# Optimization experiments

Measured on AMD Instinct MI355X. Metric: run time of the kernel, lower is better.

The kernel has to match this reference:

```python
import jax, jax.numpy as jnp
import numpy as np

N, E, D, ETYPES = 20000, 200000, 256, 16

def _gelu(x):
    return jax.nn.gelu(x, approximate=False)

def setup_inputs() -> dict:
    key = jax.random.key(0)
    ks = jax.random.split(key, 24)
    s = lambda k, shape, fan: (jax.random.normal(k, shape, jnp.float32) / np.sqrt(fan)).astype(jnp.float32)
    inp = {}
    inp['node_embeddings'] = jax.random.normal(ks[0], (N, D), jnp.float32)
    inp['edge_index'] = jax.random.randint(ks[1], (2, E), 0, N, jnp.int64 if jax.config.jax_enable_x64 else jnp.int32)
    inp['edge_type'] = jax.random.randint(ks[2], (E,), 0, ETYPES, jnp.int32)
    inp['task_embedding'] = jax.random.normal(ks[3], (D,), jnp.float32)
    inp['edge_emb'] = s(ks[4], (ETYPES, D), D)
    inp['msg_W'] = s(ks[5], (D, D), D); inp['msg_b'] = jnp.zeros((D,), jnp.float32)
    inp['att_W1'] = s(ks[6], (4 * D, D), 4 * D); inp['att_b1'] = jnp.zeros((D,), jnp.float32)
    inp['att_W2'] = s(ks[7], (D, 1), D); inp['att_b2'] = jnp.zeros((1,), jnp.float32)
    inp['edge_scale'] = jnp.asarray(0.5, jnp.float32)
    inp['ma_W1'] = s(ks[8], (D, 2 * D), D); inp['ma_b1'] = jnp.zeros((2 * D,), jnp.float32)
    inp['ma_W2'] = s(ks[9], (2 * D, 2 * D), 2 * D); inp['ma_b2'] = jnp.zeros((2 * D,), jnp.float32)
    inp['up_W1'] = s(ks[10], (2 * D, D), 2 * D); inp['up_b1'] = jnp.zeros((D,), jnp.float32)
    inp['up_W2'] = s(ks[11], (D, D), D); inp['up_b2'] = jnp.zeros((D,), jnp.float32)
    inp['ua_W1'] = s(ks[12], (D, 2 * D), D); inp['ua_b1'] = jnp.zeros((2 * D,), jnp.float32)
    inp['ua_W2'] = s(ks[13], (2 * D, 2 * D), 2 * D); inp['ua_b2'] = jnp.zeros((2 * D,), jnp.float32)
    inp['ln_g'] = jnp.ones((D,), jnp.float32); inp['ln_b'] = jnp.zeros((D,), jnp.float32)
    return inp

def reference(node_embeddings, edge_index, edge_type, task_embedding, edge_emb,
              msg_W, msg_b, att_W1, att_b1, att_W2, att_b2, edge_scale,
              ma_W1, ma_b1, ma_W2, ma_b2, up_W1, up_b1, up_W2, up_b2,
              ua_W1, ua_b1, ua_W2, ua_b2, ln_g, ln_b):
    n_nodes = node_embeddings.shape[0]
    src, dst = edge_index[0], edge_index[1]
    e = edge_emb[edge_type]                       # [E, D]
    x_src = node_embeddings[src]                  # [E, D]
    x_dst = node_embeddings[dst]                  # [E, D]
    messages = (x_src + e) @ msg_W + msg_b        # [E, D]
    # edge attention over [x_src, x_dst, edge_repr, task]
    task_rep = jnp.broadcast_to(task_embedding, (src.shape[0], task_embedding.shape[0]))
    att_in = jnp.concatenate([x_src, x_dst, e, task_rep], axis=-1)  # [E, 4D]
    edge_delta = jnp.tanh(_gelu(att_in @ att_W1 + att_b1) @ att_W2 + att_b2)  # [E, 1]
    edge_weight = 1.0 + edge_scale * edge_delta   # [E, 1]
    # FiLM-style message adapter from task embedding
    ma = _gelu(task_embedding @ ma_W1 + ma_b1) @ ma_W2 + ma_b2      # [2D]
    msg_gamma, msg_beta = ma[:ma.shape[0] // 2], ma[ma.shape[0] // 2:]
    messages = messages * (1.0 + 0.5 * jnp.tanh(msg_gamma)) + msg_beta
    messages = messages * edge_weight
    # scatter-add aggregation with degree normalization
    agg = jax.ops.segment_sum(messages, dst, num_segments=n_nodes)            # [N, D]
    deg = jax.ops.segment_sum(edge_weight[:, 0], dst, num_segments=n_nodes)   # [N]
    agg = agg / jnp.maximum(deg, 1.0)[:, None]
    ua = _gelu(task_embedding @ ua_W1 + ua_b1) @ ua_W2 + ua_b2      # [2D]
    upd_gamma, upd_beta = ua[:ua.shape[0] // 2], ua[ua.shape[0] // 2:]
    agg = agg * (1.0 + 0.5 * jnp.tanh(upd_gamma)) + upd_beta
    upd_in = jnp.concatenate([node_embeddings, agg], axis=-1)       # [N, 2D]
    updated = _gelu(upd_in @ up_W1 + up_b1) @ up_W2 + up_b2         # [N, D]
    y = node_embeddings + updated
    mu = jnp.mean(y, axis=-1, keepdims=True)
    var = jnp.mean((y - mu) ** 2, axis=-1, keepdims=True)
    return (y - mu) / jnp.sqrt(var + 1e-5) * ln_g + ln_b
```

## Files before the change

### kernel.cpp

```cpp
#include <hip/hip_runtime.h>
#include <hip/hip_bf16.h>

#define NN 20000
#define NE 200000

typedef __bf16 bf16x8 __attribute__((ext_vector_type(8)));
typedef float f32x4 __attribute__((ext_vector_type(4)));
typedef unsigned short u16x8 __attribute__((ext_vector_type(8)));

constexpr int TAB_MSG_SCALE = 0;
constexpr int TAB_MSG_BETA  = 256;
constexpr int TAB_UPD_SCALE = 512;
constexpr int TAB_UPD_BETA  = 768;
constexpr int TAB_TASKC     = 1024;
constexpr int TAB_ECM       = 1280;
constexpr size_t OFF_WPRET = 40960;
constexpr size_t OFF_W1T   = 434176;
constexpr size_t OFF_W2T   = 696320;
constexpr size_t OFF_CNT   = 827392;
constexpr size_t OFF_SRCET = 907392;
constexpr size_t OFF_UPDB  = 11147392;
constexpr size_t OFF_G     = 21387392;
constexpr size_t OFF_P2B   = 41867392;
constexpr size_t WS_NEED   = 52107392;

constexpr int ROW_BLOCKS = (NN + 63)/64;

__device__ __forceinline__ float bf2f(unsigned short u){
  union { unsigned int i; float f; } v; v.i = ((unsigned int)u) << 16; return v.f;
}
__device__ __forceinline__ unsigned short f2bf(float f){
  __bf16 h = (__bf16)f; unsigned short u; __builtin_memcpy(&u, &h, 2); return u;
}
__device__ __forceinline__ float gelu_f(float x){
  return 0.5f * x * (1.0f + erff(x * 0.70710678118654752f));
}
__device__ __forceinline__ float gelu_fast(float x){
  return x / (1.0f + __expf(-1.702f * x));
}
__device__ __forceinline__ float tanh_fast(float x){
  float e = __expf(2.0f * x);
  return 1.0f - 2.0f / (e + 1.0f);
}
__device__ __forceinline__ float sum16(const float* p){
  float a = ((p[0]+p[1])+(p[2]+p[3])) + ((p[4]+p[5])+(p[6]+p[7]));
  float b = ((p[8]+p[9])+(p[10]+p[11])) + ((p[12]+p[13])+(p[14]+p[15]));
  return a + b;
}

__global__ __launch_bounds__(256) void k_setup(
    const float* __restrict__ task, const float* __restrict__ eemb,
    const float* __restrict__ msg_W, const float* __restrict__ msg_b,
    const float* __restrict__ att_W1, const float* __restrict__ att_b1,
    const float* __restrict__ ma_W1, const float* __restrict__ ma_b1,
    const float* __restrict__ ma_W2, const float* __restrict__ ma_b2,
    const float* __restrict__ ua_W1, const float* __restrict__ ua_b1,
    const float* __restrict__ ua_W2, const float* __restrict__ ua_b2,
    const float* __restrict__ up_W1, const float* __restrict__ up_W2,
    const int* __restrict__ eidx, const int* __restrict__ etype,
    float* __restrict__ tabs,
    unsigned short* __restrict__ WpreT, unsigned short* __restrict__ W1T,
    unsigned short* __restrict__ W2T, int* __restrict__ cnt,
    unsigned int* __restrict__ srcet)
{
  __shared__ float s_in[512];
  __shared__ float s_h[512];
  int bb = blockIdx.x, tid = threadIdx.x;
  if (bb >= 1315){
    int e = (bb - 1315)*256 + tid;
    if (e < NE){
      int dst = eidx[NE + e];
      int pos = atomicAdd(&cnt[dst], 1);
      srcet[((unsigned)dst << 7) + pos] =
          (unsigned int)eidx[e] | ((unsigned int)etype[e] << 16);
    }
    return;
  }
  if (bb >= 35){
    int b = bb - 35;
    if (b < 768){
      int n = b;
      float v;
      if (n < 256)      v = msg_W[tid*256 + n];
      else if (n < 512) v = att_W1[tid*256 + (n - 256)];
      else              v = att_W1[(256 + tid)*256 + (n - 512)];
      WpreT[n*256 + tid] = f2bf(v);
    } else if (b < 1024){
      int n = b - 768;
      W1T[n*512 + tid]       = f2bf(up_W1[tid*256 + n]);
      W1T[n*512 + 256 + tid] = f2bf(up_W1[(256 + tid)*256 + n]);
    } else {
      int n = b - 1024;
      W2T[n*256 + tid] = f2bf(up_W2[tid*256 + n]);
    }
    return;
  }
  int b = bb;
  if (b < 2){
    const float* W1 = b ? ua_W1 : ma_W1;  const float* b1 = b ? ua_b1 : ma_b1;
    const float* W2 = b ? ua_W2 : ma_W2;  const float* b2 = b ? ua_b2 : ma_b2;
    s_in[tid] = task[tid];
    __syncthreads();
    #pragma unroll
    for (int jj = 0; jj < 2; ++jj){
      int j = tid + jj*256;
      float pacc[16];
      #pragma unroll
      for (int u = 0; u < 16; ++u) pacc[u] = 0.f;
      for (int k0 = 0; k0 < 256; k0 += 16){
        float wv[16];
        #pragma unroll
        for (int u = 0; u < 16; ++u) wv[u] = W1[(k0 + u)*512 + j];
        #pragma unroll
        for (int u = 0; u < 16; ++u) pacc[u] += s_in[k0 + u] * wv[u];
      }
      s_h[j] = gelu_f(b1[j] + sum16(pacc));
    }
    __syncthreads();
    float o[2];
    #pragma unroll
    for (int jj = 0; jj < 2; ++jj){
      int j = tid + jj*256;
      float pacc[16];
      #pragma unroll
      for (int u = 0; u < 16; ++u) pacc[u] = 0.f;
      for (int k0 = 0; k0 < 512; k0 += 16){
        float wv[16];
        #pragma unroll
        for (int u = 0; u < 16; ++u) wv[u] = W2[(k0 + u)*512 + j];
        #pragma unroll
        for (int u = 0; u < 16; ++u) pacc[u] += s_h[k0 + u] * wv[u];
      }
      o[jj] = b2[j] + sum16(pacc);
    }
    float* scale = tabs + (b ? TAB_UPD_SCALE : TAB_MSG_SCALE);
    float* beta  = tabs + (b ? TAB_UPD_BETA  : TAB_MSG_BETA);
    scale[tid] = 1.0f + 0.5f * tanhf(o[0]);
    beta[tid]  = o[1];
  } else if (b == 2){
    s_in[tid] = task[tid];
    __syncthreads();
    float pacc[16];
    #pragma unroll
    for (int u = 0; u < 16; ++u) pacc[u] = 0.f;
    for (int k0 = 0; k0 < 256; k0 += 16){
      float wv[16];
      #pragma unroll
      for (int u = 0; u < 16; ++u) wv[u] = att_W1[(768 + k0 + u)*256 + tid];
      #pragma unroll
      for (int u = 0; u < 16; ++u) pacc[u] += s_in[k0 + u] * wv[u];
    }
    tabs[TAB_TASKC + tid] = att_b1[tid] + sum16(pacc);
  } else if (b < 19){
    int t = b - 3;
    s_in[tid] = eemb[t*256 + tid];
    __syncthreads();
    float pacc[16];
    #pragma unroll
    for (int u = 0; u < 16; ++u) pacc[u] = 0.f;
    for (int k0 = 0; k0 < 256; k0 += 16){
      float wv[16];
      #pragma unroll
      for (int u = 0; u < 16; ++u) wv[u] = msg_W[(k0 + u)*256 + tid];
      #pragma unroll
      for (int u = 0; u < 16; ++u) pacc[u] += s_in[k0 + u] * wv[u];
    }
    tabs[TAB_ECM + t*512 + ((tid >> 2) << 3) + 4 + (tid & 3)] = msg_b[tid] + sum16(pacc);
  } else {
    int t = b - 19;
    s_in[tid] = eemb[t*256 + tid];
    __syncthreads();
    float pacc[16];
    #pragma unroll
    for (int u = 0; u < 16; ++u) pacc[u] = 0.f;
    for (int k0 = 0; k0 < 256; k0 += 16){
      float wv[16];
      #pragma unroll
      for (int u = 0; u < 16; ++u) wv[u] = att_W1[(512 + k0 + u)*256 + tid];
      #pragma unroll
      for (int u = 0; u < 16; ++u) pacc[u] += s_in[k0 + u] * wv[u];
    }
    tabs[TAB_ECM + t*512 + ((tid >> 2) << 3) + (tid & 3)] = sum16(pacc);
  }
}

__global__ __launch_bounds__(256) void k_gemm_pre(
    const float* __restrict__ X, const unsigned short* __restrict__ WpreT,
    const float* __restrict__ tabs,
    unsigned short* __restrict__ G, unsigned short* __restrict__ P2b)
{
  __shared__ __align__(16) unsigned short s_b[16*256];
  int tid = threadIdx.x;
  int bb = blockIdx.x;
  int rb = bb >> 2, chunk = bb & 3;
  int wv = tid >> 6, lane = tid & 63;
  int m0 = rb*64 + wv*16;
  bool valid = (m0 < NN);
  int lo = lane & 15, hi = lane >> 4;
  bf16x8 a[8];
  if (valid){
    const float* xrow = X + (size_t)(m0 + lo)*256 + hi*8;
    #pragma unroll
    for (int kc = 0; kc < 8; ++kc){
      float4 f0 = *(const float4*)(xrow + kc*32);
      float4 f1 = *(const float4*)(xrow + kc*32 + 4);
      bf16x8 v;
      v[0]=(__bf16)f0.x; v[1]=(__bf16)f0.y; v[2]=(__bf16)f0.z; v[3]=(__bf16)f0.w;
      v[4]=(__bf16)f1.x; v[5]=(__bf16)f1.y; v[6]=(__bf16)f1.z; v[7]=(__bf16)f1.w;
      a[kc] = v;
    }
  }
  int sn = tid >> 4, sk0 = (tid & 15)*16;
  int sswz = (sn & 7) << 3;
  int rswz = (lo & 7) << 3;
  for (int t = 0; t < 12; ++t){
    int nt = chunk*12 + t;
    __syncthreads();
    {
      const unsigned short* gsrc = WpreT + (size_t)(nt*16 + sn)*256 + sk0;
      uint4 d0 = *(const uint4*)(gsrc);
      uint4 d1 = *(const uint4*)(gsrc + 8);
      *(uint4*)(s_b + sn*256 + (sk0 ^ sswz))       = d0;
      *(uint4*)(s_b + sn*256 + ((sk0 + 8) ^ sswz)) = d1;
    }
    __syncthreads();
    if (!valid) continue;
    f32x4 acc = {0.f, 0.f, 0.f, 0.f};
    #pragma unroll
    for (int kc = 0; kc < 8; ++kc){
      bf16x8 bfrag = *(const bf16x8*)(s_b + lo*256 + ((kc*32 + hi*8) ^ rswz));
      acc = __builtin_amdgcn_mfma_f32_16x16x32_bf16(a[kc], bfrag, acc, 0, 0, 0);
    }
    int n0 = nt*16;
    if (nt < 16){
      int j = n0 + lo;
      unsigned short* grow = G + (size_t)(m0 + hi*4)*512 + 256 + j;
      #pragma unroll
      for (int r = 0; r < 4; ++r) grow[(size_t)r*512] = f2bf(acc[r]);
    } else if (nt < 32){
      int j = n0 - 256 + lo;
      unsigned short* grow = G + (size_t)(m0 + hi*4)*512 + j;
      #pragma unroll
      for (int r = 0; r < 4; ++r) grow[(size_t)r*512] = f2bf(acc[r]);
    } else {
      int j = n0 - 512 + lo;
      float tcadd = tabs[TAB_TASKC + j];
      unsigned short* prow = P2b + (size_t)(m0 + hi*4)*256 + j;
      #pragma unroll
      for (int r = 0; r < 4; ++r) prow[(size_t)r*256] = f2bf(acc[r] + tcadd);
    }
  }
}

__global__ __launch_bounds__(256) void k_agg(
    const int* __restrict__ cnt, const unsigned int* __restrict__ srcet,
    const unsigned short* __restrict__ G, const unsigned short* __restrict__ P2b,
    const float* __restrict__ tabs, const float* __restrict__ attW2,
    const float* __restrict__ attb2, const float* __restrict__ escale,
    unsigned short* __restrict__ updB)
{
  int wv = threadIdx.x >> 6, lane = threadIdx.x & 63;
  int h = lane >> 5, l = lane & 31;
  int node = blockIdx.x*8 + wv*2 + h;
  int d0 = l*8;
  float sc = escale[0], bb = attb2[0];

  float q[8], w2v[8];
  {
    u16x8 p2 = *(const u16x8*)(P2b + (size_t)node*256 + d0);
    #pragma unroll
    for (int j = 0; j < 8; ++j) q[j] = bf2f(p2[j]);
    float4 wa = *(const float4*)(attW2 + d0);
    float4 wb = *(const float4*)(attW2 + d0 + 4);
    w2v[0]=wa.x; w2v[1]=wa.y; w2v[2]=wa.z; w2v[3]=wa.w;
    w2v[4]=wb.x; w2v[5]=wb.y; w2v[6]=wb.z; w2v[7]=wb.w;
  }
  const float* ecm_base = tabs + TAB_ECM + (l << 4);

  int start = node << 7;
  int end = start + cnt[node];
  float acc[8];
  #pragma unroll
  for (int j = 0; j < 8; ++j) acc[j] = 0.f;
  float W = 0.f;

  unsigned int se0 = 0, se1 = 0;
  u16x8 p1a = {0,0,0,0,0,0,0,0}, mma = {0,0,0,0,0,0,0,0};
  if (start < end){
    se0 = srcet[start];
    const unsigned short* gr = G + (((unsigned)(se0 & 0xFFFFu)) << 9);
    p1a = *(const u16x8*)(gr + d0);
    mma = *(const u16x8*)(gr + 256 + d0);
    if (start + 1 < end) se1 = srcet[start + 1];
  }
  for (int i = start; i < end; ++i){
    u16x8 p1b = p1a, mmb = mma;
    unsigned int se2 = 0;
    if (i + 1 < end){
      const unsigned short* gr = G + (((unsigned)(se1 & 0xFFFFu)) << 9);
      p1b = *(const u16x8*)(gr + d0);
      mmb = *(const u16x8*)(gr + 256 + d0);
    }
    if (i + 2 < end) se2 = srcet[i + 2];
    int et = (int)(se0 >> 16);
    const float* ecm = ecm_base + (et << 9);
    float4 ec0 = *(const float4*)(ecm);
    float4 em0 = *(const float4*)(ecm + 4);
    float4 ec1 = *(const float4*)(ecm + 8);
    float4 em1 = *(const float4*)(ecm + 12);
    float part =
        gelu_fast(bf2f(p1a[0]) + q[0] + ec0.x)*w2v[0]
      + gelu_fast(bf2f(p1a[1]) + q[1] + ec0.y)*w2v[1]
      + gelu_fast(bf2f(p1a[2]) + q[2] + ec0.z)*w2v[2]
      + gelu_fast(bf2f(p1a[3]) + q[3] + ec0.w)*w2v[3]
      + gelu_fast(bf2f(p1a[4]) + q[4] + ec1.x)*w2v[4]
      + gelu_fast(bf2f(p1a[5]) + q[5] + ec1.y)*w2v[5]
      + gelu_fast(bf2f(p1a[6]) + q[6] + ec1.z)*w2v[6]
      + gelu_fast(bf2f(p1a[7]) + q[7] + ec1.w)*w2v[7];
    part += __shfl_xor(part, 1);
    part += __shfl_xor(part, 2);
    part += __shfl_xor(part, 4);
    part += __shfl_xor(part, 8);
    part += __shfl_xor(part, 16);
    float w = 1.0f + sc*tanh_fast(part + bb);
    acc[0] += w*(bf2f(mma[0]) + em0.x);
    acc[1] += w*(bf2f(mma[1]) + em0.y);
    acc[2] += w*(bf2f(mma[2]) + em0.z);
    acc[3] += w*(bf2f(mma[3]) + em0.w);
    acc[4] += w*(bf2f(mma[4]) + em1.x);
    acc[5] += w*(bf2f(mma[5]) + em1.y);
    acc[6] += w*(bf2f(mma[6]) + em1.z);
    acc[7] += w*(bf2f(mma[7]) + em1.w);
    W += w;
    se0 = se1; se1 = se2; p1a = p1b; mma = mmb;
  }

  float d = fmaxf(W, 1.0f), rd = 1.0f / d;
  unsigned short st[8];
  #pragma unroll
  for (int c = 0; c < 2; ++c){
    float4 ms = *(const float4*)(tabs + TAB_MSG_SCALE + d0 + c*4);
    float4 mb = *(const float4*)(tabs + TAB_MSG_BETA  + d0 + c*4);
    float4 us = *(const float4*)(tabs + TAB_UPD_SCALE + d0 + c*4);
    float4 ub = *(const float4*)(tabs + TAB_UPD_BETA  + d0 + c*4);
    st[c*4+0] = f2bf((ms.x*acc[c*4+0] + mb.x*W)*rd*us.x + ub.x);
    st[c*4+1] = f2bf((ms.y*acc[c*4+1] + mb.y*W)*rd*us.y + ub.y);
    st[c*4+2] = f2bf((ms.z*acc[c*4+2] + mb.z*W)*rd*us.z + ub.z);
    st[c*4+3] = f2bf((ms.w*acc[c*4+3] + mb.w*W)*rd*us.w + ub.w);
  }
  *(u16x8*)(updB + (size_t)node*256 + d0) = *(u16x8*)(st);
}

__device__ __forceinline__ bf16x8 ldA(const float* xrow, const unsigned short* urow, int ke){
  if (ke < 256){
    float4 f0 = *(const float4*)(xrow + ke);
    float4 f1 = *(const float4*)(xrow + ke + 4);
    bf16x8 v;
    v[0]=(__bf16)f0.x; v[1]=(__bf16)f0.y; v[2]=(__bf16)f0.z; v[3]=(__bf16)f0.w;
    v[4]=(__bf16)f1.x; v[5]=(__bf16)f1.y; v[6]=(__bf16)f1.z; v[7]=(__bf16)f1.w;
    return v;
  }
  return *(const bf16x8*)(urow + (ke - 256));
}

__global__ __launch_bounds__(256) void k_mlp(
    const float* __restrict__ X, const unsigned short* __restrict__ updB,
    const unsigned short* __restrict__ W1T, const unsigned short* __restrict__ W2T,
    const float* __restrict__ up_b1, const float* __restrict__ up_b2,
    const float* __restrict__ ln_g, const float* __restrict__ ln_b,
    float* __restrict__ out)
{
  __shared__ __align__(16) unsigned short s_H[32*256];
  __shared__ float s_sum[4*32], s_sq[4*32];
  __shared__ float s_mu[32], s_rs[32];
  int m0 = blockIdx.x*32;
  int tid = threadIdx.x;
  int wv = tid >> 6, lane = tid & 63, lo = lane & 15, hi = lane >> 4;

  const float* x0 = X + (size_t)(m0 + lo)*256;
  const float* x1 = x0 + 16*256;
  const unsigned short* u0 = updB + (size_t)(m0 + lo)*256;
  const unsigned short* u1 = u0 + 16*256;

  f32x4 acc0[4], acc1[4];
  #pragma unroll
  for (int t = 0; t < 4; ++t){
    float b = up_b1[wv*64 + t*16 + lo];
    acc0[t] = (f32x4){b, b, b, b};
    acc1[t] = acc0[t];
  }
  #pragma unroll
  for (int kc = 0; kc < 16; ++kc){
    int ke = kc*32 + hi*8;
    bf16x8 a0 = ldA(x0, u0, ke);
    bf16x8 a1 = ldA(x1, u1, ke);
    #pragma unroll
    for (int t = 0; t < 4; ++t){
      int n = wv*64 + t*16 + lo;
      bf16x8 bf = *(const bf16x8*)(W1T + (size_t)n*512 + ke);
      acc0[t] = __builtin_amdgcn_mfma_f32_16x16x32_bf16(a0, bf, acc0[t], 0, 0, 0);
      acc1[t] = __builtin_amdgcn_mfma_f32_16x16x32_bf16(a1, bf, acc1[t], 0, 0, 0);
    }
  }
  #pragma unroll
  for (int t = 0; t < 4; ++t){
    #pragma unroll
    for (int r = 0; r < 4; ++r){
      int row0 = hi*4 + r, n = wv*64 + t*16 + lo;
      s_H[(row0 << 8) | (n ^ ((row0 & 7) << 3))] = f2bf(gelu_fast(acc0[t][r]));
      int row1 = row0 + 16;
      s_H[(row1 << 8) | (n ^ ((row1 & 7) << 3))] = f2bf(gelu_fast(acc1[t][r]));
    }
  }
  __syncthreads();

  f32x4 y0[4], y1[4];
  #pragma unroll
  for (int t = 0; t < 4; ++t){
    float b = up_b2[wv*64 + t*16 + lo];
    y0[t] = (f32x4){b, b, b, b};
    y1[t] = y0[t];
  }
  #pragma unroll
  for (int kc = 0; kc < 8; ++kc){
    int ke = kc*32 + hi*8;
    bf16x8 af0 = *(const bf16x8*)(s_H + ((lo << 8) | (ke ^ ((lo & 7) << 3))));
    int r1 = lo + 16;
    bf16x8 af1 = *(const bf16x8*)(s_H + ((r1 << 8) | (ke ^ ((r1 & 7) << 3))));
    #pragma unroll
    for (int t = 0; t < 4; ++t){
      int n = wv*64 + t*16 + lo;
      bf16x8 bf = *(const bf16x8*)(W2T + (size_t)n*256 + ke);
      y0[t] = __builtin_amdgcn_mfma_f32_16x16x32_bf16(af0, bf, y0[t], 0, 0, 0);
      y1[t] = __builtin_amdgcn_mfma_f32_16x16x32_bf16(af1, bf, y1[t], 0, 0, 0);
    }
  }

  #pragma unroll
  for (int t = 0; t < 4; ++t){
    #pragma unroll
    for (int r = 0; r < 4; ++r){
      int row0 = hi*4 + r, n = wv*64 + t*16 + lo;
      y0[t][r] += X[(size_t)(m0 + row0)*256 + n];
      y1[t][r] += X[(size_t)(m0 + row0 + 16)*256 + n];
    }
  }

  float ps[2][4], pq[2][4];
  #pragma unroll
  for (int r = 0; r < 4; ++r){
    float s0 = 0.f, q0 = 0.f, s1 = 0.f, q1 = 0.f;
    #pragma unroll
    for (int t = 0; t < 4; ++t){
      s0 += y0[t][r]; q0 += y0[t][r]*y0[t][r];
      s1 += y1[t][r]; q1 += y1[t][r]*y1[t][r];
    }
    #pragma unroll
    for (int off = 1; off < 16; off <<= 1){
      s0 += __shfl_xor(s0, off); q0 += __shfl_xor(q0, off);
      s1 += __shfl_xor(s1, off); q1 += __shfl_xor(q1, off);
    }
    ps[0][r] = s0; pq[0][r] = q0;
    ps[1][r] = s1; pq[1][r] = q1;
  }
  if (lo == 0){
    #pragma unroll
    for (int m = 0; m < 2; ++m){
      #pragma unroll
      for (int r = 0; r < 4; ++r){
        int row = m*16 + hi*4 + r;
        s_sum[wv*32 + row] = ps[m][r];
        s_sq [wv*32 + row] = pq[m][r];
      }
    }
  }
  __syncthreads();
  if (tid < 32){
    float sum = s_sum[tid] + s_sum[32 + tid] + s_sum[64 + tid] + s_sum[96 + tid];
    float sq  = s_sq[tid]  + s_sq[32 + tid]  + s_sq[64 + tid]  + s_sq[96 + tid];
    float mu = sum * (1.0f/256.0f);
    float var = sq * (1.0f/256.0f) - mu*mu;
    s_mu[tid] = mu;
    s_rs[tid] = rsqrtf(var + 1e-5f);
  }
  __syncthreads();

  #pragma unroll
  for (int t = 0; t < 4; ++t){
    int n = wv*64 + t*16 + lo;
    float lg = ln_g[n], lb = ln_b[n];
    #pragma unroll
    for (int r = 0; r < 4; ++r){
      int row0 = hi*4 + r, row1 = row0 + 16;
      out[(size_t)(m0 + row0)*256 + n] = (y0[t][r] - s_mu[row0]) * s_rs[row0] * lg + lb;
      out[(size_t)(m0 + row1)*256 + n] = (y1[t][r] - s_mu[row1]) * s_rs[row1] * lg + lb;
    }
  }
}

extern "C" void kernel_launch(void* const* d_in, const int* in_sizes, int n_in,
                              void* d_out, int out_size, void* d_ws, size_t ws_size,
                              hipStream_t stream)
{
  (void)in_sizes; (void)n_in; (void)out_size;
  if (ws_size < WS_NEED) return;
  const float* X      = (const float*)d_in[0];
  const int*   eidx   = (const int*)d_in[1];
  const int*   etype  = (const int*)d_in[2];
  const float* task   = (const float*)d_in[3];
  const float* eemb   = (const float*)d_in[4];
  const float* msg_W  = (const float*)d_in[5];
  const float* msg_b  = (const float*)d_in[6];
  const float* att_W1 = (const float*)d_in[7];
  const float* att_b1 = (const float*)d_in[8];
  const float* att_W2 = (const float*)d_in[9];
  const float* att_b2 = (const float*)d_in[10];
  const float* escale = (const float*)d_in[11];
  const float* ma_W1  = (const float*)d_in[12];
  const float* ma_b1  = (const float*)d_in[13];
  const float* ma_W2  = (const float*)d_in[14];
  const float* ma_b2  = (const float*)d_in[15];
  const float* up_W1  = (const float*)d_in[16];
  const float* up_b1  = (const float*)d_in[17];
  const float* up_W2  = (const float*)d_in[18];
  const float* up_b2  = (const float*)d_in[19];
  const float* ua_W1  = (const float*)d_in[20];
  const float* ua_b1  = (const float*)d_in[21];
  const float* ua_W2  = (const float*)d_in[22];
  const float* ua_b2  = (const float*)d_in[23];
  const float* ln_g   = (const float*)d_in[24];
  const float* ln_b   = (const float*)d_in[25];
  char* ws = (char*)d_ws;
  float* tabs = (float*)ws;
  unsigned short* WpreT = (unsigned short*)(ws + OFF_WPRET);
  unsigned short* W1T   = (unsigned short*)(ws + OFF_W1T);
  unsigned short* W2T   = (unsigned short*)(ws + OFF_W2T);
  int*          cnt   = (int*)(ws + OFF_CNT);
  unsigned int* srcet = (unsigned int*)(ws + OFF_SRCET);
  unsigned short* updB = (unsigned short*)(ws + OFF_UPDB);
  unsigned short* G    = (unsigned short*)(ws + OFF_G);
  unsigned short* P2b  = (unsigned short*)(ws + OFF_P2B);
  float* out = (float*)d_out;

  hipMemsetAsync(cnt, 0, (size_t)NN*4, stream);
  k_setup<<<2097, 256, 0, stream>>>(task, eemb, msg_W, msg_b, att_W1, att_b1,
                                    ma_W1, ma_b1, ma_W2, ma_b2,
                                    ua_W1, ua_b1, ua_W2, ua_b2,
                                    up_W1, up_W2, eidx, etype,
                                    tabs, WpreT, W1T, W2T, cnt, srcet);
  k_gemm_pre<<<ROW_BLOCKS*4, 256, 0, stream>>>(X, WpreT, tabs, G, P2b);
  k_agg<<<NN/8, 256, 0, stream>>>(cnt, srcet, G, P2b, tabs,
                                  att_W2, att_b2, escale, updB);
  k_mlp<<<NN/32, 256, 0, stream>>>(X, updB, W1T, W2T, up_b1, up_b2,
                                   ln_g, ln_b, out);
}
```

Before: 194.3 us.

## Fold pre-GEMM into setup kernel, reading fp32 weights directly

```diff
diff --git a/kernel.cpp b/kernel.cpp
--- a/kernel.cpp
+++ b/kernel.cpp
@@ -14,7 +14,6 @@
 constexpr int TAB_UPD_BETA  = 768;
 constexpr int TAB_TASKC     = 1024;
 constexpr int TAB_ECM       = 1280;
-constexpr size_t OFF_WPRET = 40960;
 constexpr size_t OFF_W1T   = 434176;
 constexpr size_t OFF_W2T   = 696320;
 constexpr size_t OFF_CNT   = 827392;
@@ -25,6 +24,10 @@
 constexpr size_t WS_NEED   = 52107392;
 
 constexpr int ROW_BLOCKS = (NN + 63)/64;
+constexpr int SB_PREP = 35;
+constexpr int SB_CSR  = 547;
+constexpr int SB_GEMM = 1329;
+constexpr int SB_TOTAL = 2581;
 
 __device__ __forceinline__ float bf2f(unsigned short u){
   union { unsigned int i; float f; } v; v.i = ((unsigned int)u) << 16; return v.f;
@@ -58,16 +61,83 @@
     const float* __restrict__ ua_W2, const float* __restrict__ ua_b2,
     const float* __restrict__ up_W1, const float* __restrict__ up_W2,
     const int* __restrict__ eidx, const int* __restrict__ etype,
+    const float* __restrict__ X,
     float* __restrict__ tabs,
-    unsigned short* __restrict__ WpreT, unsigned short* __restrict__ W1T,
-    unsigned short* __restrict__ W2T, int* __restrict__ cnt,
-    unsigned int* __restrict__ srcet)
+    unsigned short* __restrict__ W1T, unsigned short* __restrict__ W2T,
+    int* __restrict__ cnt, unsigned int* __restrict__ srcet,
+    unsigned short* __restrict__ G, unsigned short* __restrict__ P2b)
 {
-  __shared__ float s_in[512];
-  __shared__ float s_h[512];
+  __shared__ __align__(16) unsigned char smem[8192];
   int bb = blockIdx.x, tid = threadIdx.x;
-  if (bb >= 1315){
-    int e = (bb - 1315)*256 + tid;
+
+  if (bb >= SB_GEMM){
+    unsigned short* s_b = (unsigned short*)smem;
+    int g = bb - SB_GEMM;
+    int rb = g >> 2, chunk = g & 3;
+    int wv = tid >> 6, lane = tid & 63;
+    int m0 = rb*64 + wv*16;
+    bool valid = (m0 < NN);
+    int lo = lane & 15, hi = lane >> 4;
+    bf16x8 a[8];
+    if (valid){
+      const float* xrow = X + (size_t)(m0 + lo)*256 + hi*8;
+      #pragma unroll
+      for (int kc = 0; kc < 8; ++kc){
+        float4 f0 = *(const float4*)(xrow + kc*32);
+        float4 f1 = *(const float4*)(xrow + kc*32 + 4);
+        bf16x8 v;
+        v[0]=(__bf16)f0.x; v[1]=(__bf16)f0.y; v[2]=(__bf16)f0.z; v[3]=(__bf16)f0.w;
+        v[4]=(__bf16)f1.x; v[5]=(__bf16)f1.y; v[6]=(__bf16)f1.z; v[7]=(__bf16)f1.w;
+        a[kc] = v;
+      }
+    }
+    int sn = tid >> 4, sk0 = (tid & 15)*16;
+    int sswz = (sn & 7) << 3;
+    int rswz = (lo & 7) << 3;
+    for (int t = 0; t < 12; ++t){
+      int nt = chunk*12 + t;
+      __syncthreads();
+      {
+        int cn = nt*16 + sn;
+        const float* col;
+        if (cn < 256)      col = msg_W + cn;
+        else if (cn < 512) col = att_W1 + (cn - 256);
+        else               col = att_W1 + 256*256 + (cn - 512);
+        #pragma unroll
+        for (int u = 0; u < 16; ++u)
+          s_b[sn*256 + ((sk0 + u) ^ sswz)] = f2bf(col[(size_t)(sk0 + u)*256]);
+      }
+      __syncthreads();
+      if (!valid) continue;
+      f32x4 acc = {0.f, 0.f, 0.f, 0.f};
+      #pragma unroll
+      for (int kc = 0; kc < 8; ++kc){
+        bf16x8 bfrag = *(const bf16x8*)(s_b + lo*256 + ((kc*32 + hi*8) ^ rswz));
+        acc = __builtin_amdgcn_mfma_f32_16x16x32_bf16(a[kc], bfrag, acc, 0, 0, 0);
+      }
+      int n0 = nt*16;
+      if (nt < 16){
+        int j = n0 + lo;
+        unsigned short* grow = G + (size_t)(m0 + hi*4)*512 + 256 + j;
+        #pragma unroll
+        for (int r = 0; r < 4; ++r) grow[(size_t)r*512] = f2bf(acc[r]);
+      } else if (nt < 32){
+        int j = n0 - 256 + lo;
+        unsigned short* grow = G + (size_t)(m0 + hi*4)*512 + j;
+        #pragma unroll
+        for (int r = 0; r < 4; ++r) grow[(size_t)r*512] = f2bf(acc[r]);
+      } else {
+        int j = n0 - 512 + lo;
+        unsigned short* prow = P2b + (size_t)(m0 + hi*4)*256 + j;
+        #pragma unroll
+        for (int r = 0; r < 4; ++r) prow[(size_t)r*256] = f2bf(acc[r]);
+      }
+    }
+    return;
+  }
+
+  if (bb >= SB_CSR){
+    int e = (bb - SB_CSR)*256 + tid;
     if (e < NE){
       int dst = eidx[NE + e];
       int pos = atomicAdd(&cnt[dst], 1);
@@ -76,25 +146,22 @@
     }
     return;
   }
-  if (bb >= 35){
-    int b = bb - 35;
-    if (b < 768){
-      int n = b;
-      float v;
-      if (n < 256)      v = msg_W[tid*256 + n];
-      else if (n < 512) v = att_W1[tid*256 + (n - 256)];
-      else              v = att_W1[(256 + tid)*256 + (n - 512)];
-      WpreT[n*256 + tid] = f2bf(v);
-    } else if (b < 1024){
-      int n = b - 768;
+
+  if (bb >= SB_PREP){
+    int p = bb - SB_PREP;
+    if (p < 256){
+      int n = p;
       W1T[n*512 + tid]       = f2bf(up_W1[tid*256 + n]);
       W1T[n*512 + 256 + tid] = f2bf(up_W1[(256 + tid)*256 + n]);
     } else {
-      int n = b - 1024;
+      int n = p - 256;
       W2T[n*256 + tid] = f2bf(up_W2[tid*256 + n]);
     }
     return;
   }
+
+  float* s_in = (float*)smem;
+  float* s_h  = (float*)(smem + 2048);
   int b = bb;
   if (b < 2){
     const float* W1 = b ? ua_W1 : ma_W1;  const float* b1 = b ? ua_b1 : ma_b1;
@@ -181,74 +248,6 @@
       for (int u = 0; u < 16; ++u) pacc[u] += s_in[k0 + u] * wv[u];
     }
     tabs[TAB_ECM + t*512 + ((tid >> 2) << 3) + (tid & 3)] = sum16(pacc);
-  }
-}
-
-__global__ __launch_bounds__(256) void k_gemm_pre(
-    const float* __restrict__ X, const unsigned short* __restrict__ WpreT,
-    const float* __restrict__ tabs,
-    unsigned short* __restrict__ G, unsigned short* __restrict__ P2b)
-{
-  __shared__ __align__(16) unsigned short s_b[16*256];
-  int tid = threadIdx.x;
-  int bb = blockIdx.x;
-  int rb = bb >> 2, chunk = bb & 3;
-  int wv = tid >> 6, lane = tid & 63;
-  int m0 = rb*64 + wv*16;
-  bool valid = (m0 < NN);
-  int lo = lane & 15, hi = lane >> 4;
-  bf16x8 a[8];
-  if (valid){
-    const float* xrow = X + (size_t)(m0 + lo)*256 + hi*8;
-    #pragma unroll
-    for (int kc = 0; kc < 8; ++kc){
-      float4 f0 = *(const float4*)(xrow + kc*32);
-      float4 f1 = *(const float4*)(xrow + kc*32 + 4);
-      bf16x8 v;
-      v[0]=(__bf16)f0.x; v[1]=(__bf16)f0.y; v[2]=(__bf16)f0.z; v[3]=(__bf16)f0.w;
-      v[4]=(__bf16)f1.x; v[5]=(__bf16)f1.y; v[6]=(__bf16)f1.z; v[7]=(__bf16)f1.w;
-      a[kc] = v;
-    }
-  }
-  int sn = tid >> 4, sk0 = (tid & 15)*16;
-  int sswz = (sn & 7) << 3;
-  int rswz = (lo & 7) << 3;
-  for (int t = 0; t < 12; ++t){
-    int nt = chunk*12 + t;
-    __syncthreads();
-    {
-      const unsigned short* gsrc = WpreT + (size_t)(nt*16 + sn)*256 + sk0;
-      uint4 d0 = *(const uint4*)(gsrc);
-      uint4 d1 = *(const uint4*)(gsrc + 8);
-      *(uint4*)(s_b + sn*256 + (sk0 ^ sswz))       = d0;
-      *(uint4*)(s_b + sn*256 + ((sk0 + 8) ^ sswz)) = d1;
-    }
-    __syncthreads();
-    if (!valid) continue;
-    f32x4 acc = {0.f, 0.f, 0.f, 0.f};
-    #pragma unroll
-    for (int kc = 0; kc < 8; ++kc){
-      bf16x8 bfrag = *(const bf16x8*)(s_b + lo*256 + ((kc*32 + hi*8) ^ rswz));
-      acc = __builtin_amdgcn_mfma_f32_16x16x32_bf16(a[kc], bfrag, acc, 0, 0, 0);
-    }
-    int n0 = nt*16;
-    if (nt < 16){
-      int j = n0 + lo;
-      unsigned short* grow = G + (size_t)(m0 + hi*4)*512 + 256 + j;
-      #pragma unroll
-      for (int r = 0; r < 4; ++r) grow[(size_t)r*512] = f2bf(acc[r]);
-    } else if (nt < 32){
-      int j = n0 - 256 + lo;
-      unsigned short* grow = G + (size_t)(m0 + hi*4)*512 + j;
-      #pragma unroll
-      for (int r = 0; r < 4; ++r) grow[(size_t)r*512] = f2bf(acc[r]);
-    } else {
-      int j = n0 - 512 + lo;
-      float tcadd = tabs[TAB_TASKC + j];
-      unsigned short* prow = P2b + (size_t)(m0 + hi*4)*256 + j;
-      #pragma unroll
-      for (int r = 0; r < 4; ++r) prow[(size_t)r*256] = f2bf(acc[r] + tcadd);
-    }
   }
 }
 
@@ -268,8 +267,12 @@
   float q[8], w2v[8];
   {
     u16x8 p2 = *(const u16x8*)(P2b + (size_t)node*256 + d0);
-    #pragma unroll
-    for (int j = 0; j < 8; ++j) q[j] = bf2f(p2[j]);
+    float4 t0 = *(const float4*)(tabs + TAB_TASKC + d0);
+    float4 t1 = *(const float4*)(tabs + TAB_TASKC + d0 + 4);
+    q[0] = bf2f(p2[0]) + t0.x; q[1] = bf2f(p2[1]) + t0.y;
+    q[2] = bf2f(p2[2]) + t0.z; q[3] = bf2f(p2[3]) + t0.w;
+    q[4] = bf2f(p2[4]) + t1.x; q[5] = bf2f(p2[5]) + t1.y;
+    q[6] = bf2f(p2[6]) + t1.z; q[7] = bf2f(p2[7]) + t1.w;
     float4 wa = *(const float4*)(attW2 + d0);
     float4 wb = *(const float4*)(attW2 + d0 + 4);
     w2v[0]=wa.x; w2v[1]=wa.y; w2v[2]=wa.z; w2v[3]=wa.w;
@@ -532,7 +535,6 @@
   const float* ln_b   = (const float*)d_in[25];
   char* ws = (char*)d_ws;
   float* tabs = (float*)ws;
-  unsigned short* WpreT = (unsigned short*)(ws + OFF_WPRET);
   unsigned short* W1T   = (unsigned short*)(ws + OFF_W1T);
   unsigned short* W2T   = (unsigned short*)(ws + OFF_W2T);
   int*          cnt   = (int*)(ws + OFF_CNT);
@@ -543,12 +545,11 @@
   float* out = (float*)d_out;
 
   hipMemsetAsync(cnt, 0, (size_t)NN*4, stream);
-  k_setup<<<2097, 256, 0, stream>>>(task, eemb, msg_W, msg_b, att_W1, att_b1,
-                                    ma_W1, ma_b1, ma_W2, ma_b2,
-                                    ua_W1, ua_b1, ua_W2, ua_b2,
-                                    up_W1, up_W2, eidx, etype,
-                                    tabs, WpreT, W1T, W2T, cnt, srcet);
-  k_gemm_pre<<<ROW_BLOCKS*4, 256, 0, stream>>>(X, WpreT, tabs, G, P2b);
+  k_setup<<<SB_TOTAL, 256, 0, stream>>>(task, eemb, msg_W, msg_b, att_W1, att_b1,
+                                        ma_W1, ma_b1, ma_W2, ma_b2,
+                                        ua_W1, ua_b1, ua_W2, ua_b2,
+                                        up_W1, up_W2, eidx, etype, X,
+                                        tabs, W1T, W2T, cnt, srcet, G, P2b);
   k_agg<<<NN/8, 256, 0, stream>>>(cnt, srcet, G, P2b, tabs,
                                   att_W2, att_b2, escale, updB);
   k_mlp<<<NN/32, 256, 0, stream>>>(X, updB, W1T, W2T, up_b1, up_b2,
```

Measured after the change: 287.9 us. +48.1%, slower.
